# Kernel optimization log

Hardware: AMD Instinct MI355X
Metric: run time of the kernel (lower is better)

Reference implementation:

```python
import jax, jax.numpy as jnp
import numpy as np

# Fixed architecture constants (hardcoded in PPGEncoder)
B_DEF, C_IN, L_SEQ = 64, 4, 256
H, N_STATE, N_BLOCKS = 4, 4, 2  # d_model, SSM state size, n_blocks


def _layernorm(v, scale, bias, eps=1e-5):
    mu = v.mean(-1, keepdims=True)
    var = v.var(-1, keepdims=True)
    return (v - mu) / jnp.sqrt(var + eps) * scale + bias


def _avgpool1d(v, out_size):
    # AdaptiveAvgPool1d where out_size divides L evenly -> block mean
    b, c, l = v.shape
    return v.reshape(b, c, out_size, l // out_size).mean(-1)


def setup_inputs() -> dict:
    key = jax.random.key(0)
    ks = iter(jax.random.split(key, 40))
    nrm = lambda shape, s=1.0: jax.random.normal(next(ks), shape, jnp.float32) * s
    inp = {
        "x": nrm((B_DEF, C_IN, L_SEQ)),
        # S4 encoder / decoder linears
        "enc_W": nrm((C_IN, H), 0.5), "enc_b": jnp.zeros((H,), jnp.float32),
        # per-block S4D params, stacked over blocks
        "ln_s": jnp.ones((N_BLOCKS, H), jnp.float32), "ln_b": jnp.zeros((N_BLOCKS, H), jnp.float32),
        "log_dt": jax.random.uniform(next(ks), (N_BLOCKS, H), jnp.float32,
                                      minval=float(np.log(1e-3)), maxval=float(np.log(1e-1))),
        "A_re": nrm((N_BLOCKS, H, N_STATE), 0.5),
        "A_im": jnp.tile(jnp.pi * jnp.arange(N_STATE, dtype=jnp.float32), (N_BLOCKS, H, 1)),
        "C_re": nrm((N_BLOCKS, H, N_STATE), 0.5), "C_im": nrm((N_BLOCKS, H, N_STATE), 0.5),
        "D": nrm((N_BLOCKS, H), 1.0),
        "out_W": nrm((N_BLOCKS, H, H), 0.5), "out_b": jnp.zeros((N_BLOCKS, H), jnp.float32),
        "dec_W": nrm((H, H), 0.5), "dec_b": jnp.zeros((H,), jnp.float32),
        # projection MLP: Linear(1856,1024) LN ReLU Linear(1024,4096) LN ReLU Unflatten(512,8) Linear(8,4096)
        "W1": nrm((1856, 1024), 0.02), "b1": jnp.zeros((1024,), jnp.float32),
        "g1": jnp.ones((1024,), jnp.float32), "be1": jnp.zeros((1024,), jnp.float32),
        "W2": nrm((1024, 4096), 0.02), "b2": jnp.zeros((4096,), jnp.float32),
        "g2": jnp.ones((4096,), jnp.float32), "be2": jnp.zeros((4096,), jnp.float32),
        "W3": nrm((8, 4096), 0.3), "b3": jnp.zeros((4096,), jnp.float32),
    }
    return inp


def _s4_model(x, enc_W, enc_b, ln_s, ln_b, log_dt, A_re, A_im, C_re, C_im, D,
              out_W, out_b, dec_W, dec_b):
    # x: [B, C_IN, L]; S4Model consumes [B, L, d_input]
    L = x.shape[-1]
    u = jnp.einsum('bcl,ch->blh', x, enc_W) + enc_b  # [B,L,H]
    t = jnp.arange(L, dtype=jnp.float32)
    for i in range(ln_s.shape[0]):
        z = _layernorm(u, ln_s[i], ln_b[i])          # prenorm
        zc = jnp.swapaxes(z, 1, 2)                   # [B,H,L]
        dt = jnp.exp(log_dt[i])                      # [H]
        A = -jnp.exp(A_re[i]) + 1j * A_im[i]         # stable diag SSM [H,N]
        dtA = A * dt[:, None]
        Bd = (jnp.exp(dtA) - 1.0) / A                # ZOH input discretization
        C = C_re[i] + 1j * C_im[i]
        vand = jnp.exp(dtA[:, :, None] * t)          # [H,N,L] Vandermonde
        K = 2.0 * jnp.real(jnp.einsum('hn,hnl->hl', C * Bd, vand))  # [H,L]
        # causal FFT convolution + skip D
        Uf = jnp.fft.rfft(zc, n=2 * L)
        Kf = jnp.fft.rfft(K, n=2 * L)
        y = jnp.fft.irfft(Uf * Kf, n=2 * L)[..., :L] + D[i][:, None] * zc
        y = jax.nn.gelu(y)
        y = jnp.einsum('bhl,hk->blk', y, out_W[i]) + out_b[i]
        u = u + y                                    # residual
    return u @ dec_W + dec_b                         # [B,L,H]


def reference(x, enc_W, enc_b, ln_s, ln_b, log_dt, A_re, A_im, C_re, C_im, D,
              out_W, out_b, dec_W, dec_b, W1, b1, g1, be1, W2, b2, g2, be2, W3, b3):
    b = x.shape[0]
    s4_out = _s4_model(x, enc_W, enc_b, ln_s, ln_b, log_dt, A_re, A_im,
                       C_re, C_im, D, out_W, out_b, dec_W, dec_b)  # [B,L,H]
    zc = jnp.swapaxes(s4_out, 1, 2)                  # [B,H,L]
    z16 = _avgpool1d(zc, 16)                         # [B,4,16]
    # FeaturePyramidPooling on raw x: sizes 64,128,256
    fpp = jnp.concatenate([_avgpool1d(x, 64), _avgpool1d(x, 128), _avgpool1d(x, 256)], axis=-1)
    combined = jnp.concatenate([z16.reshape(b, -1), fpp.reshape(b, -1)], axis=1)  # [B,1856]
    h = jax.nn.relu(_layernorm(combined @ W1 + b1, g1, be1))   # [B,1024] (dropout=eval identity)
    h = jax.nn.relu(_layernorm(h @ W2 + b2, g2, be2))          # [B,4096]
    h = h.reshape(b, 512, 8)
    return h @ W3 + b3                                         # [B,512,4096]
```

## Files before the change

### kernel.cpp

```cpp
#include <hip/hip_runtime.h>
#include <hip/hip_bf16.h>
#include <math.h>

#define BDEF 64
#define LSEQ 256
#define HD   4
#define NST  4
#define NBLK 2

typedef float nfloat4 __attribute__((ext_vector_type(4)));

__device__ inline void nt_store4(const float4 v, float* p) {
    nfloat4 nv = {v.x, v.y, v.z, v.w};
    __builtin_nontemporal_store(nv, (nfloat4*)p);
}

__global__ __launch_bounds__(256) void s4front(
    const float* __restrict__ x, const float* __restrict__ enc_W,
    const float* __restrict__ enc_b, const float* __restrict__ ln_s,
    const float* __restrict__ ln_b, const float* __restrict__ log_dt,
    const float* __restrict__ A_re, const float* __restrict__ A_im,
    const float* __restrict__ C_re, const float* __restrict__ C_im,
    const float* __restrict__ Dp, const float* __restrict__ out_W,
    const float* __restrict__ out_b, const float* __restrict__ dec_W,
    const float* __restrict__ dec_b, float* __restrict__ combined)
{
    const int b = blockIdx.x;
    const int l = threadIdx.x;
    __shared__ float Kl[NBLK][LSEQ][4];
    __shared__ float x_lds[4][256];
    __shared__ float z_lds[256][4];
    __shared__ float s4_lds[256][4];

    {
        const float t = (float)l;
        for (int i = 0; i < NBLK; ++i) {
            #pragma unroll
            for (int h = 0; h < HD; ++h) {
                float dt = expf(log_dt[i*HD + h]);
                float acc = 0.f;
                #pragma unroll
                for (int n = 0; n < NST; ++n) {
                    const int idx = (i*HD + h)*NST + n;
                    float ar = -expf(A_re[idx]);
                    float ai = A_im[idx];
                    float dr = ar*dt, di = ai*dt;
                    float er  = expf(dr);
                    float e1r = er*cosf(di) - 1.0f;
                    float e1i = er*sinf(di);
                    float inv = 1.0f/(ar*ar + ai*ai);
                    float bdr = (e1r*ar + e1i*ai)*inv;
                    float bdi = (e1i*ar - e1r*ai)*inv;
                    float cr = C_re[idx], ci = C_im[idx];
                    float cbr = cr*bdr - ci*bdi;
                    float cbi = cr*bdi + ci*bdr;
                    float em = expf(dr*t);
                    float vr = em*cosf(di*t);
                    float vi = em*sinf(di*t);
                    acc += cbr*vr - cbi*vi;
                }
                Kl[i][l][h] = 2.0f*acc;
            }
        }
    }

    #pragma unroll
    for (int c = 0; c < 4; ++c)
        x_lds[c][l] = x[(b*4 + c)*256 + l];

    float u[4];
    #pragma unroll
    for (int h = 0; h < 4; ++h) {
        float a = enc_b[h];
        #pragma unroll
        for (int c = 0; c < 4; ++c) a += x_lds[c][l]*enc_W[c*4 + h];
        u[h] = a;
    }
    __syncthreads();

    for (int i = 0; i < NBLK; ++i) {
        float mu = 0.25f*(u[0]+u[1]+u[2]+u[3]);
        float var = 0.f;
        #pragma unroll
        for (int h = 0; h < 4; ++h) { float d = u[h]-mu; var += d*d; }
        var *= 0.25f;
        float rs = rsqrtf(var + 1e-5f);
        float z[4];
        #pragma unroll
        for (int h = 0; h < 4; ++h)
            z[h] = (u[h]-mu)*rs*ln_s[i*4 + h] + ln_b[i*4 + h];
        *(float4*)&z_lds[l][0] = make_float4(z[0], z[1], z[2], z[3]);
        __syncthreads();

        float y0 = 0.f, y1 = 0.f, y2 = 0.f, y3 = 0.f;
        const int mlim = l | 63;
        #pragma unroll 4
        for (int m = 0; m <= mlim; ++m) {
            float4 kk = *(const float4*)&Kl[i][m][0];
            int p = (l - m) & 255;
            float4 zz = *(const float4*)&z_lds[p][0];
            if (m <= l) {
                y0 += kk.x*zz.x; y1 += kk.y*zz.y;
                y2 += kk.z*zz.z; y3 += kk.w*zz.w;
            }
        }
        float y[4] = {y0, y1, y2, y3};
        #pragma unroll
        for (int h = 0; h < 4; ++h) {
            float v = y[h] + Dp[i*4 + h]*z[h];
            float inner = 0.7978845608028654f*(v + 0.044715f*v*v*v);
            y[h] = 0.5f*v*(1.0f + tanhf(inner));
        }
        #pragma unroll
        for (int k = 0; k < 4; ++k) {
            float a = out_b[i*4 + k];
            #pragma unroll
            for (int h = 0; h < 4; ++h) a += y[h]*out_W[(i*4 + h)*4 + k];
            u[k] += a;
        }
        __syncthreads();
    }

    #pragma unroll
    for (int h = 0; h < 4; ++h) {
        float a = dec_b[h];
        #pragma unroll
        for (int k = 0; k < 4; ++k) a += u[k]*dec_W[k*4 + h];
        s4_lds[l][h] = a;
    }
    __syncthreads();

    float* cmb = combined + b*1856;
    if (l < 64) {
        int h = l >> 4, kk = l & 15;
        float a = 0.f;
        #pragma unroll
        for (int j = 0; j < 16; ++j) a += s4_lds[kk*16 + j][h];
        cmb[l] = a*(1.0f/16.0f);
    }
    for (int e = l; e < 1792; e += 256) {
        int c = e/448, jj = e%448;
        float v;
        if (jj < 64) {
            v = 0.25f*(x_lds[c][4*jj] + x_lds[c][4*jj+1] +
                       x_lds[c][4*jj+2] + x_lds[c][4*jj+3]);
        } else if (jj < 192) {
            int q = jj - 64;
            v = 0.5f*(x_lds[c][2*q] + x_lds[c][2*q+1]);
        } else {
            v = x_lds[c][jj - 192];
        }
        cmb[64 + e] = v;
    }
}

template<int NCOLS, int ASTRIDE, int KCH>
__global__ __launch_bounds__(256) void mlp_part(
    const float* __restrict__ A, const float* __restrict__ W,
    float* __restrict__ parts)
{
    __shared__ float At[64][KCH + 4];
    __shared__ float Wl[KCH][64];
    const int ks = blockIdx.x, k0 = ks*KCH;
    const int j0 = blockIdx.y*64;
    const int t  = threadIdx.x;

    {
        constexpr int AF4 = 64*KCH/4;
        constexpr int RF4 = KCH/4;
        #pragma unroll
        for (int f = t; f < AF4; f += 256) {
            const int row = f / RF4, c4 = f % RF4;
            *(float4*)&At[row][c4*4] =
                *(const float4*)(A + (size_t)row*ASTRIDE + k0 + c4*4);
        }
        constexpr int WF4 = KCH*16;
        #pragma unroll
        for (int f = t; f < WF4; f += 256) {
            const int row = f >> 4, c4 = f & 15;
            *(float4*)&Wl[row][c4*4] =
                *(const float4*)(W + (size_t)(k0 + row)*NCOLS + j0 + c4*4);
        }
    }
    __syncthreads();

    const int bi = t >> 4, ji = t & 15;
    const int br = bi*4;
    float4 acc0 = {0,0,0,0}, acc1 = {0,0,0,0}, acc2 = {0,0,0,0}, acc3 = {0,0,0,0};
    #pragma unroll 8
    for (int k = 0; k < KCH; ++k) {
        float4 wv = *(const float4*)&Wl[k][ji*4];
        float a0 = At[br+0][k], a1 = At[br+1][k];
        float a2 = At[br+2][k], a3 = At[br+3][k];
        acc0.x += a0*wv.x; acc0.y += a0*wv.y; acc0.z += a0*wv.z; acc0.w += a0*wv.w;
        acc1.x += a1*wv.x; acc1.y += a1*wv.y; acc1.z += a1*wv.z; acc1.w += a1*wv.w;
        acc2.x += a2*wv.x; acc2.y += a2*wv.y; acc2.z += a2*wv.z; acc2.w += a2*wv.w;
        acc3.x += a3*wv.x; acc3.y += a3*wv.y; acc3.z += a3*wv.z; acc3.w += a3*wv.w;
    }
    float* pbase = parts + (size_t)(ks*64 + br)*NCOLS + j0 + ji*4;
    *(float4*)(pbase)             = acc0;
    *(float4*)(pbase + NCOLS)     = acc1;
    *(float4*)(pbase + 2*NCOLS)   = acc2;
    *(float4*)(pbase + 3*NCOLS)   = acc3;
}

template<int N>
__global__ __launch_bounds__(256) void reduce_ln_relu(
    const float* __restrict__ parts, const float* __restrict__ bias,
    const float* __restrict__ g, const float* __restrict__ be,
    float* __restrict__ out, int KS)
{
    constexpr int NV = N/1024;
    const int b = blockIdx.x, t = threadIdx.x;
    float4 acc[NV];
    #pragma unroll
    for (int v = 0; v < NV; ++v)
        acc[v] = *(const float4*)(bias + v*1024 + t*4);
    for (int ks = 0; ks < KS; ++ks) {
        const float* p = parts + (size_t)(ks*64 + b)*N;
        #pragma unroll
        for (int v = 0; v < NV; ++v) {
            float4 q = *(const float4*)(p + v*1024 + t*4);
            acc[v].x += q.x; acc[v].y += q.y; acc[v].z += q.z; acc[v].w += q.w;
        }
    }
    float s = 0.f, s2 = 0.f;
    #pragma unroll
    for (int v = 0; v < NV; ++v) {
        s  += acc[v].x + acc[v].y + acc[v].z + acc[v].w;
        s2 += acc[v].x*acc[v].x + acc[v].y*acc[v].y +
              acc[v].z*acc[v].z + acc[v].w*acc[v].w;
    }
    #pragma unroll
    for (int off = 32; off > 0; off >>= 1) {
        s  += __shfl_down(s,  off);
        s2 += __shfl_down(s2, off);
    }
    __shared__ float red[2][4];
    const int w = t >> 6;
    if ((t & 63) == 0) { red[0][w] = s; red[1][w] = s2; }
    __syncthreads();
    float ts  = red[0][0] + red[0][1] + red[0][2] + red[0][3];
    float ts2 = red[1][0] + red[1][1] + red[1][2] + red[1][3];
    const float inv_n = 1.0f/(float)N;
    float mu  = ts*inv_n;
    float var = ts2*inv_n - mu*mu;
    float rs  = rsqrtf(var + 1e-5f);
    #pragma unroll
    for (int v = 0; v < NV; ++v) {
        const int j = v*1024 + t*4;
        float4 gv  = *(const float4*)(g + j);
        float4 bev = *(const float4*)(be + j);
        float4 o;
        o.x = fmaxf((acc[v].x - mu)*rs*gv.x + bev.x, 0.f);
        o.y = fmaxf((acc[v].y - mu)*rs*gv.y + bev.y, 0.f);
        o.z = fmaxf((acc[v].z - mu)*rs*gv.z + bev.z, 0.f);
        o.w = fmaxf((acc[v].w - mu)*rs*gv.w + bev.w, 0.f);
        *(float4*)(out + (size_t)b*N + j) = o;
    }
}

#define ROWS_D 64
__global__ __launch_bounds__(256) void final_mm(
    const float* __restrict__ h2, const float* __restrict__ W3,
    const float* __restrict__ b3, float* __restrict__ out)
{
    const int rg = blockIdx.x;
    const int js = blockIdx.y;
    const int t  = threadIdx.x;
    const int bs0 = rg*ROWS_D;
    const int j = js*1024 + t*4;
    float4 w[8];
    #pragma unroll
    for (int k = 0; k < 8; ++k) w[k] = *(const float4*)(W3 + k*4096 + j);
    const float4 bv = *(const float4*)(b3 + j);
    const float* __restrict__ hrow = h2 + (size_t)bs0*8;
    float* __restrict__ obase = out + (size_t)bs0*4096 + j;
    #pragma unroll 4
    for (int r = 0; r < ROWS_D; ++r) {
        float4 acc = bv;
        #pragma unroll
        for (int k = 0; k < 8; ++k) {
            const float hv = hrow[r*8 + k];
            acc.x += hv*w[k].x; acc.y += hv*w[k].y;
            acc.z += hv*w[k].z; acc.w += hv*w[k].w;
        }
        nt_store4(acc, obase + (size_t)r*4096);
    }
}

extern "C" void kernel_launch(void* const* d_in, const int* in_sizes, int n_in,
                              void* d_out, int out_size, void* d_ws, size_t ws_size,
                              hipStream_t stream) {
    const float* x      = (const float*)d_in[0];
    const float* enc_W  = (const float*)d_in[1];
    const float* enc_b  = (const float*)d_in[2];
    const float* ln_s   = (const float*)d_in[3];
    const float* ln_b   = (const float*)d_in[4];
    const float* log_dt = (const float*)d_in[5];
    const float* A_re   = (const float*)d_in[6];
    const float* A_im   = (const float*)d_in[7];
    const float* C_re   = (const float*)d_in[8];
    const float* C_im   = (const float*)d_in[9];
    const float* Dp     = (const float*)d_in[10];
    const float* out_W  = (const float*)d_in[11];
    const float* out_b  = (const float*)d_in[12];
    const float* dec_W  = (const float*)d_in[13];
    const float* dec_b  = (const float*)d_in[14];
    const float* W1     = (const float*)d_in[15];
    const float* b1     = (const float*)d_in[16];
    const float* g1     = (const float*)d_in[17];
    const float* be1    = (const float*)d_in[18];
    const float* W2     = (const float*)d_in[19];
    const float* b2     = (const float*)d_in[20];
    const float* g2     = (const float*)d_in[21];
    const float* be2    = (const float*)d_in[22];
    const float* W3     = (const float*)d_in[23];
    const float* b3     = (const float*)d_in[24];
    float* out = (float*)d_out;

    float* ws = (float*)d_ws;
    float* combined = ws;
    float* parts1   = combined + 64*1856;
    float* h1       = parts1 + 29*64*1024;
    float* parts2   = h1 + 64*1024;
    float* h2       = parts2 + 8*64*4096;

    s4front<<<64, 256, 0, stream>>>(x, enc_W, enc_b, ln_s, ln_b, log_dt,
                                    A_re, A_im, C_re, C_im, Dp,
                                    out_W, out_b, dec_W, dec_b, combined);
    mlp_part<1024,1856,64><<<dim3(29,16), 256, 0, stream>>>(combined, W1, parts1);
    reduce_ln_relu<1024><<<64, 256, 0, stream>>>(parts1, b1, g1, be1, h1, 29);
    mlp_part<4096,1024,128><<<dim3(8,64), 256, 0, stream>>>(h1, W2, parts2);
    reduce_ln_relu<4096><<<64, 256, 0, stream>>>(parts2, b2, g2, be2, h2, 8);
    final_mm<<<dim3(512,4), 256, 0, stream>>>(h2, W3, b3, out);
}
```

Before: 187.7 us.

## Fuse all stages into one cooperative persistent kernel with grid syncs

Replaces the six separate kernel launches with a single cooperative kernel of 512 blocks that runs the S4 front end, both MLP layers with their LayerNorm reductions, and the final projection as phases separated by grid.sync. The aim is to remove inter-kernel launch gaps and tail effects. The second matmul now uses 16 K-splits of 64 instead of 8 of 128, and the inner loops read float4 from LDS for both operands. A fallback to the multi-kernel path runs if occupancy or the cooperative launch fails. Risks are grid-sync overhead, phases where most blocks sit idle, and a larger parts2 buffer.

```diff
diff --git a/kernel.cpp b/kernel.cpp
--- a/kernel.cpp
+++ b/kernel.cpp
@@ -1,12 +1,8 @@
 #include <hip/hip_runtime.h>
-#include <hip/hip_bf16.h>
+#include <hip/hip_cooperative_groups.h>
 #include <math.h>
 
-#define BDEF 64
-#define LSEQ 256
-#define HD   4
-#define NST  4
-#define NBLK 2
+namespace cg = cooperative_groups;
 
 typedef float nfloat4 __attribute__((ext_vector_type(4)));
 
@@ -15,35 +11,38 @@
     __builtin_nontemporal_store(nv, (nfloat4*)p);
 }
 
-__global__ __launch_bounds__(256) void s4front(
-    const float* __restrict__ x, const float* __restrict__ enc_W,
-    const float* __restrict__ enc_b, const float* __restrict__ ln_s,
-    const float* __restrict__ ln_b, const float* __restrict__ log_dt,
-    const float* __restrict__ A_re, const float* __restrict__ A_im,
-    const float* __restrict__ C_re, const float* __restrict__ C_im,
-    const float* __restrict__ Dp, const float* __restrict__ out_W,
-    const float* __restrict__ out_b, const float* __restrict__ dec_W,
-    const float* __restrict__ dec_b, float* __restrict__ combined)
-{
-    const int b = blockIdx.x;
-    const int l = threadIdx.x;
-    __shared__ float Kl[NBLK][LSEQ][4];
-    __shared__ float x_lds[4][256];
-    __shared__ float z_lds[256][4];
-    __shared__ float s4_lds[256][4];
+struct KArgs {
+    const float *x, *enc_W, *enc_b, *ln_s, *ln_b, *log_dt, *A_re, *A_im,
+                *C_re, *C_im, *Dp, *out_W, *out_b, *dec_W, *dec_b,
+                *W1, *b1, *g1, *be1, *W2, *b2, *g2, *be2, *W3, *b3;
+    float *combined, *parts1, *h1, *parts2, *h2, *out;
+};
+
+#define ACCROW(accv, av)                                        \
+    accv.x += av.x*w0.x + av.y*w1.x + av.z*w2.x + av.w*w3.x;    \
+    accv.y += av.x*w0.y + av.y*w1.y + av.z*w2.y + av.w*w3.y;    \
+    accv.z += av.x*w0.z + av.y*w1.z + av.z*w2.z + av.w*w3.z;    \
+    accv.w += av.x*w0.w + av.y*w1.w + av.z*w2.w + av.w*w3.w;
+
+__device__ inline void s4_phase(const KArgs& a, int b, int l, float* smem)
+{
+    float* Kl  = smem;
+    float* xl  = smem + 2048;
+    float* zl  = smem + 3072;
+    float* s4l = smem + 4096;
 
     {
-        const float t = (float)l;
-        for (int i = 0; i < NBLK; ++i) {
+        const float tt = (float)l;
+        for (int i = 0; i < 2; ++i) {
             #pragma unroll
-            for (int h = 0; h < HD; ++h) {
-                float dt = expf(log_dt[i*HD + h]);
+            for (int h = 0; h < 4; ++h) {
+                float dt = expf(a.log_dt[i*4 + h]);
                 float acc = 0.f;
                 #pragma unroll
-                for (int n = 0; n < NST; ++n) {
-                    const int idx = (i*HD + h)*NST + n;
-                    float ar = -expf(A_re[idx]);
-                    float ai = A_im[idx];
+                for (int n = 0; n < 4; ++n) {
+                    const int idx = (i*4 + h)*4 + n;
+                    float ar = -expf(a.A_re[idx]);
+                    float ai = a.A_im[idx];
                     float dr = ar*dt, di = ai*dt;
                     float er  = expf(dr);
                     float e1r = er*cosf(di) - 1.0f;
@@ -51,34 +50,34 @@
                     float inv = 1.0f/(ar*ar + ai*ai);
                     float bdr = (e1r*ar + e1i*ai)*inv;
                     float bdi = (e1i*ar - e1r*ai)*inv;
-                    float cr = C_re[idx], ci = C_im[idx];
+                    float cr = a.C_re[idx], ci = a.C_im[idx];
                     float cbr = cr*bdr - ci*bdi;
                     float cbi = cr*bdi + ci*bdr;
-                    float em = expf(dr*t);
-                    float vr = em*cosf(di*t);
-                    float vi = em*sinf(di*t);
+                    float em = expf(dr*tt);
+                    float vr = em*cosf(di*tt);
+                    float vi = em*sinf(di*tt);
                     acc += cbr*vr - cbi*vi;
                 }
-                Kl[i][l][h] = 2.0f*acc;
+                Kl[(i*256 + l)*4 + h] = 2.0f*acc;
             }
         }
     }
 
     #pragma unroll
     for (int c = 0; c < 4; ++c)
-        x_lds[c][l] = x[(b*4 + c)*256 + l];
+        xl[c*256 + l] = a.x[(b*4 + c)*256 + l];
 
     float u[4];
     #pragma unroll
     for (int h = 0; h < 4; ++h) {
-        float a = enc_b[h];
-        #pragma unroll
-        for (int c = 0; c < 4; ++c) a += x_lds[c][l]*enc_W[c*4 + h];
-        u[h] = a;
-    }
-    __syncthreads();
-
-    for (int i = 0; i < NBLK; ++i) {
+        float acc = a.enc_b[h];
+        #pragma unroll
+        for (int c = 0; c < 4; ++c) acc += xl[c*256 + l]*a.enc_W[c*4 + h];
+        u[h] = acc;
+    }
+    __syncthreads();
+
+    for (int i = 0; i < 2; ++i) {
         float mu = 0.25f*(u[0]+u[1]+u[2]+u[3]);
         float var = 0.f;
         #pragma unroll
@@ -88,17 +87,17 @@
         float z[4];
         #pragma unroll
         for (int h = 0; h < 4; ++h)
-            z[h] = (u[h]-mu)*rs*ln_s[i*4 + h] + ln_b[i*4 + h];
-        *(float4*)&z_lds[l][0] = make_float4(z[0], z[1], z[2], z[3]);
+            z[h] = (u[h]-mu)*rs*a.ln_s[i*4 + h] + a.ln_b[i*4 + h];
+        *(float4*)&zl[l*4] = make_float4(z[0], z[1], z[2], z[3]);
         __syncthreads();
 
         float y0 = 0.f, y1 = 0.f, y2 = 0.f, y3 = 0.f;
         const int mlim = l | 63;
         #pragma unroll 4
         for (int m = 0; m <= mlim; ++m) {
-            float4 kk = *(const float4*)&Kl[i][m][0];
+            float4 kk = *(float4*)&Kl[(i*256 + m)*4];
             int p = (l - m) & 255;
-            float4 zz = *(const float4*)&z_lds[p][0];
+            float4 zz = *(float4*)&zl[p*4];
             if (m <= l) {
                 y0 += kk.x*zz.x; y1 += kk.y*zz.y;
                 y2 += kk.z*zz.z; y3 += kk.w*zz.w;
@@ -107,111 +106,105 @@
         float y[4] = {y0, y1, y2, y3};
         #pragma unroll
         for (int h = 0; h < 4; ++h) {
-            float v = y[h] + Dp[i*4 + h]*z[h];
+            float v = y[h] + a.Dp[i*4 + h]*z[h];
             float inner = 0.7978845608028654f*(v + 0.044715f*v*v*v);
             y[h] = 0.5f*v*(1.0f + tanhf(inner));
         }
         #pragma unroll
         for (int k = 0; k < 4; ++k) {
-            float a = out_b[i*4 + k];
+            float acc = a.out_b[i*4 + k];
             #pragma unroll
-            for (int h = 0; h < 4; ++h) a += y[h]*out_W[(i*4 + h)*4 + k];
-            u[k] += a;
+            for (int h = 0; h < 4; ++h) acc += y[h]*a.out_W[(i*4 + h)*4 + k];
+            u[k] += acc;
         }
         __syncthreads();
     }
 
     #pragma unroll
     for (int h = 0; h < 4; ++h) {
-        float a = dec_b[h];
-        #pragma unroll
-        for (int k = 0; k < 4; ++k) a += u[k]*dec_W[k*4 + h];
-        s4_lds[l][h] = a;
-    }
-    __syncthreads();
-
-    float* cmb = combined + b*1856;
+        float acc = a.dec_b[h];
+        #pragma unroll
+        for (int k = 0; k < 4; ++k) acc += u[k]*a.dec_W[k*4 + h];
+        s4l[l*4 + h] = acc;
+    }
+    __syncthreads();
+
+    float* cmb = a.combined + b*1856;
     if (l < 64) {
         int h = l >> 4, kk = l & 15;
-        float a = 0.f;
-        #pragma unroll
-        for (int j = 0; j < 16; ++j) a += s4_lds[kk*16 + j][h];
-        cmb[l] = a*(1.0f/16.0f);
+        float acc = 0.f;
+        #pragma unroll
+        for (int j = 0; j < 16; ++j) acc += s4l[(kk*16 + j)*4 + h];
+        cmb[l] = acc*(1.0f/16.0f);
     }
     for (int e = l; e < 1792; e += 256) {
         int c = e/448, jj = e%448;
         float v;
         if (jj < 64) {
-            v = 0.25f*(x_lds[c][4*jj] + x_lds[c][4*jj+1] +
-                       x_lds[c][4*jj+2] + x_lds[c][4*jj+3]);
+            v = 0.25f*(xl[c*256 + 4*jj] + xl[c*256 + 4*jj+1] +
+                       xl[c*256 + 4*jj+2] + xl[c*256 + 4*jj+3]);
         } else if (jj < 192) {
             int q = jj - 64;
-            v = 0.5f*(x_lds[c][2*q] + x_lds[c][2*q+1]);
+            v = 0.5f*(xl[c*256 + 2*q] + xl[c*256 + 2*q+1]);
         } else {
-            v = x_lds[c][jj - 192];
+            v = xl[c*256 + jj - 192];
         }
         cmb[64 + e] = v;
     }
 }
 
-template<int NCOLS, int ASTRIDE, int KCH>
-__global__ __launch_bounds__(256) void mlp_part(
-    const float* __restrict__ A, const float* __restrict__ W,
-    float* __restrict__ parts)
-{
-    __shared__ float At[64][KCH + 4];
-    __shared__ float Wl[KCH][64];
-    const int ks = blockIdx.x, k0 = ks*KCH;
-    const int j0 = blockIdx.y*64;
-    const int t  = threadIdx.x;
-
-    {
-        constexpr int AF4 = 64*KCH/4;
-        constexpr int RF4 = KCH/4;
-        #pragma unroll
-        for (int f = t; f < AF4; f += 256) {
-            const int row = f / RF4, c4 = f % RF4;
-            *(float4*)&At[row][c4*4] =
-                *(const float4*)(A + (size_t)row*ASTRIDE + k0 + c4*4);
-        }
-        constexpr int WF4 = KCH*16;
-        #pragma unroll
-        for (int f = t; f < WF4; f += 256) {
-            const int row = f >> 4, c4 = f & 15;
-            *(float4*)&Wl[row][c4*4] =
-                *(const float4*)(W + (size_t)(k0 + row)*NCOLS + j0 + c4*4);
-        }
-    }
-    __syncthreads();
-
-    const int bi = t >> 4, ji = t & 15;
-    const int br = bi*4;
-    float4 acc0 = {0,0,0,0}, acc1 = {0,0,0,0}, acc2 = {0,0,0,0}, acc3 = {0,0,0,0};
-    #pragma unroll 8
-    for (int k = 0; k < KCH; ++k) {
-        float4 wv = *(const float4*)&Wl[k][ji*4];
-        float a0 = At[br+0][k], a1 = At[br+1][k];
-        float a2 = At[br+2][k], a3 = At[br+3][k];
-        acc0.x += a0*wv.x; acc0.y += a0*wv.y; acc0.z += a0*wv.z; acc0.w += a0*wv.w;
-        acc1.x += a1*wv.x; acc1.y += a1*wv.y; acc1.z += a1*wv.z; acc1.w += a1*wv.w;
-        acc2.x += a2*wv.x; acc2.y += a2*wv.y; acc2.z += a2*wv.z; acc2.w += a2*wv.w;
-        acc3.x += a3*wv.x; acc3.y += a3*wv.y; acc3.z += a3*wv.z; acc3.w += a3*wv.w;
+template<int NCOLS, int ASTRIDE>
+__device__ inline void mlp_tile64(const float* __restrict__ A,
+                                  const float* __restrict__ W,
+                                  float* __restrict__ parts,
+                                  int ks, int jt, int t, float* smem)
+{
+    constexpr int KCH = 64, APAD = 68;
+    float* At = smem;
+    float* Wl = smem + 64*APAD;
+    const int k0 = ks*KCH, j0 = jt*64;
+    __syncthreads();
+    #pragma unroll
+    for (int f = t; f < 64*16; f += 256) {
+        const int row = f >> 4, c4 = f & 15;
+        *(float4*)&At[row*APAD + c4*4] =
+            *(const float4*)(A + (size_t)row*ASTRIDE + k0 + c4*4);
+    }
+    #pragma unroll
+    for (int f = t; f < KCH*16; f += 256) {
+        const int row = f >> 4, c4 = f & 15;
+        *(float4*)&Wl[row*64 + c4*4] =
+            *(const float4*)(W + (size_t)(k0 + row)*NCOLS + j0 + c4*4);
+    }
+    __syncthreads();
+    const int ji = t & 15, br = (t >> 4)*4;
+    float4 acc0={0,0,0,0}, acc1={0,0,0,0}, acc2={0,0,0,0}, acc3={0,0,0,0};
+    #pragma unroll 4
+    for (int k4 = 0; k4 < KCH; k4 += 4) {
+        float4 w0 = *(float4*)&Wl[(k4+0)*64 + ji*4];
+        float4 w1 = *(float4*)&Wl[(k4+1)*64 + ji*4];
+        float4 w2 = *(float4*)&Wl[(k4+2)*64 + ji*4];
+        float4 w3 = *(float4*)&Wl[(k4+3)*64 + ji*4];
+        float4 a0 = *(float4*)&At[(br+0)*APAD + k4];
+        float4 a1 = *(float4*)&At[(br+1)*APAD + k4];
+        float4 a2 = *(float4*)&At[(br+2)*APAD + k4];
+        float4 a3 = *(float4*)&At[(br+3)*APAD + k4];
+        ACCROW(acc0, a0) ACCROW(acc1, a1) ACCROW(acc2, a2) ACCROW(acc3, a3)
     }
     float* pbase = parts + (size_t)(ks*64 + br)*NCOLS + j0 + ji*4;
-    *(float4*)(pbase)             = acc0;
-    *(float4*)(pbase + NCOLS)     = acc1;
-    *(float4*)(pbase + 2*NCOLS)   = acc2;
-    *(float4*)(pbase + 3*NCOLS)   = acc3;
+    *(float4*)(pbase)           = acc0;
+    *(float4*)(pbase + NCOLS)   = acc1;
+    *(float4*)(pbase + 2*NCOLS) = acc2;
+    *(float4*)(pbase + 3*NCOLS) = acc3;
 }
 
 template<int N>
-__global__ __launch_bounds__(256) void reduce_ln_relu(
-    const float* __restrict__ parts, const float* __restrict__ bias,
-    const float* __restrict__ g, const float* __restrict__ be,
-    float* __restrict__ out, int KS)
+__device__ inline void reduce_ln_phase(const float* __restrict__ parts,
+    const float* __restrict__ bias, const float* __restrict__ g,
+    const float* __restrict__ be, float* __restrict__ out,
+    int KS, int b, int t, float* smem)
 {
     constexpr int NV = N/1024;
-    const int b = blockIdx.x, t = threadIdx.x;
     float4 acc[NV];
     #pragma unroll
     for (int v = 0; v < NV; ++v)
@@ -236,12 +229,12 @@
         s  += __shfl_down(s,  off);
         s2 += __shfl_down(s2, off);
     }
-    __shared__ float red[2][4];
+    __syncthreads();
     const int w = t >> 6;
-    if ((t & 63) == 0) { red[0][w] = s; red[1][w] = s2; }
-    __syncthreads();
-    float ts  = red[0][0] + red[0][1] + red[0][2] + red[0][3];
-    float ts2 = red[1][0] + red[1][1] + red[1][2] + red[1][3];
+    if ((t & 63) == 0) { smem[w] = s; smem[4 + w] = s2; }
+    __syncthreads();
+    float ts  = smem[0] + smem[1] + smem[2] + smem[3];
+    float ts2 = smem[4] + smem[5] + smem[6] + smem[7];
     const float inv_n = 1.0f/(float)N;
     float mu  = ts*inv_n;
     float var = ts2*inv_n - mu*mu;
@@ -260,15 +253,143 @@
     }
 }
 
-#define ROWS_D 64
+#define SMEM_F 8448
+
+__global__ __launch_bounds__(256, 2) void mega(KArgs a)
+{
+    __shared__ float smem[SMEM_F];
+    cg::grid_group grid = cg::this_grid();
+    const int blk = blockIdx.x;
+    const int t   = threadIdx.x;
+
+    if (blk < 64) s4_phase(a, blk, t, smem);
+    __threadfence();
+    grid.sync();
+
+    if (blk < 464)
+        mlp_tile64<1024, 1856>(a.combined, a.W1, a.parts1,
+                               blk % 29, blk / 29, t, smem);
+    __threadfence();
+    grid.sync();
+
+    if (blk < 64)
+        reduce_ln_phase<1024>(a.parts1, a.b1, a.g1, a.be1, a.h1, 29, blk, t, smem);
+    __threadfence();
+    grid.sync();
+
+    #pragma unroll
+    for (int it = 0; it < 2; ++it) {
+        const int tile = blk + it*512;
+        mlp_tile64<4096, 1024>(a.h1, a.W2, a.parts2,
+                               tile & 15, tile >> 4, t, smem);
+    }
+    __threadfence();
+    grid.sync();
+
+    if (blk < 64)
+        reduce_ln_phase<4096>(a.parts2, a.b2, a.g2, a.be2, a.h2, 16, blk, t, smem);
+    __threadfence();
+    grid.sync();
+
+    {
+        const int rg  = blk;
+        const int bs0 = rg*64;
+        float* h_lds = smem;
+        __syncthreads();
+        for (int e = t; e < 512; e += 256)
+            h_lds[e] = a.h2[(size_t)rg*512 + e];
+        __syncthreads();
+        for (int js = 0; js < 4; ++js) {
+            const int j = js*1024 + t*4;
+            float4 w[8];
+            #pragma unroll
+            for (int k = 0; k < 8; ++k)
+                w[k] = *(const float4*)(a.W3 + k*4096 + j);
+            const float4 bv = *(const float4*)(a.b3 + j);
+            float* __restrict__ obase = a.out + (size_t)bs0*4096 + j;
+            #pragma unroll 4
+            for (int r = 0; r < 64; ++r) {
+                float4 acc = bv;
+                #pragma unroll
+                for (int k = 0; k < 8; ++k) {
+                    const float hv = h_lds[r*8 + k];
+                    acc.x += hv*w[k].x; acc.y += hv*w[k].y;
+                    acc.z += hv*w[k].z; acc.w += hv*w[k].w;
+                }
+                nt_store4(acc, obase + (size_t)r*4096);
+            }
+        }
+    }
+}
+
+__global__ __launch_bounds__(256) void s4front(KArgs a)
+{
+    __shared__ float smem[5120];
+    s4_phase(a, blockIdx.x, threadIdx.x, smem);
+}
+
+template<int NCOLS, int ASTRIDE, int KCH>
+__global__ __launch_bounds__(256) void mlp_part(
+    const float* __restrict__ A, const float* __restrict__ W,
+    float* __restrict__ parts)
+{
+    __shared__ float At[64][KCH + 4];
+    __shared__ float Wl[KCH][64];
+    const int ks = blockIdx.x, k0 = ks*KCH;
+    const int j0 = blockIdx.y*64;
+    const int t  = threadIdx.x;
+    constexpr int AF4 = 64*KCH/4, RF4 = KCH/4;
+    #pragma unroll
+    for (int f = t; f < AF4; f += 256) {
+        const int row = f / RF4, c4 = f % RF4;
+        *(float4*)&At[row][c4*4] =
+            *(const float4*)(A + (size_t)row*ASTRIDE + k0 + c4*4);
+    }
+    constexpr int WF4 = KCH*16;
+    #pragma unroll
+    for (int f = t; f < WF4; f += 256) {
+        const int row = f >> 4, c4 = f & 15;
+        *(float4*)&Wl[row][c4*4] =
+            *(const float4*)(W + (size_t)(k0 + row)*NCOLS + j0 + c4*4);
+    }
+    __syncthreads();
+    const int ji = t & 15, br = (t >> 4)*4;
+    float4 acc0={0,0,0,0}, acc1={0,0,0,0}, acc2={0,0,0,0}, acc3={0,0,0,0};
+    #pragma unroll 4
+    for (int k4 = 0; k4 < KCH; k4 += 4) {
+        float4 w0 = *(float4*)&Wl[k4+0][ji*4];
+        float4 w1 = *(float4*)&Wl[k4+1][ji*4];
+        float4 w2 = *(float4*)&Wl[k4+2][ji*4];
+        float4 w3 = *(float4*)&Wl[k4+3][ji*4];
+        float4 a0 = *(float4*)&At[br+0][k4];
+        float4 a1 = *(float4*)&At[br+1][k4];
+        float4 a2 = *(float4*)&At[br+2][k4];
+        float4 a3 = *(float4*)&At[br+3][k4];
+        ACCROW(acc0, a0) ACCROW(acc1, a1) ACCROW(acc2, a2) ACCROW(acc3, a3)
+    }
+    float* pbase = parts + (size_t)(ks*64 + br)*NCOLS + j0 + ji*4;
+    *(float4*)(pbase)           = acc0;
+    *(float4*)(pbase + NCOLS)   = acc1;
+    *(float4*)(pbase + 2*NCOLS) = acc2;
+    *(float4*)(pbase + 3*NCOLS) = acc3;
+}
+
+template<int N>
+__global__ __launch_bounds__(256) void reduce_ln_relu(
+    const float* __restrict__ parts, const float* __restrict__ bias,
+    const float* __restrict__ g, const float* __restrict__ be,
+    float* __restrict__ out, int KS)
+{
+    __shared__ float smem[8];
+    reduce_ln_phase<N>(parts, bias, g, be, out, KS, blockIdx.x, threadIdx.x, smem);
+}
+
 __global__ __launch_bounds__(256) void final_mm(
     const float* __restrict__ h2, const float* __restrict__ W3,
     const float* __restrict__ b3, float* __restrict__ out)
 {
-    const int rg = blockIdx.x;
-    const int js = blockIdx.y;
-    const int t  = threadIdx.x;
-    const int bs0 = rg*ROWS_D;
+    const int rg = blockIdx.x, js = blockIdx.y, t = threadIdx.x;
+    const int bs0 = rg*64;
     const int j = js*1024 + t*4;
     float4 w[8];
     #pragma unroll
@@ -277,7 +398,7 @@
     const float* __restrict__ hrow = h2 + (size_t)bs0*8;
     float* __restrict__ obase = out + (size_t)bs0*4096 + j;
     #pragma unroll 4
-    for (int r = 0; r < ROWS_D; ++r) {
+    for (int r = 0; r < 64; ++r) {
         float4 acc = bv;
         #pragma unroll
         for (int k = 0; k < 8; ++k) {
@@ -292,46 +413,56 @@
 extern "C" void kernel_launch(void* const* d_in, const int* in_sizes, int n_in,
                               void* d_out, int out_size, void* d_ws, size_t ws_size,
                               hipStream_t stream) {
-    const float* x      = (const float*)d_in[0];
-    const float* enc_W  = (const float*)d_in[1];
-    const float* enc_b  = (const float*)d_in[2];
-    const float* ln_s   = (const float*)d_in[3];
-    const float* ln_b   = (const float*)d_in[4];
-    const float* log_dt = (const float*)d_in[5];
-    const float* A_re   = (const float*)d_in[6];
-    const float* A_im   = (const float*)d_in[7];
-    const float* C_re   = (const float*)d_in[8];
-    const float* C_im   = (const float*)d_in[9];
-    const float* Dp     = (const float*)d_in[10];
-    const float* out_W  = (const float*)d_in[11];
-    const float* out_b  = (const float*)d_in[12];
-    const float* dec_W  = (const float*)d_in[13];
-    const float* dec_b  = (const float*)d_in[14];
-    const float* W1     = (const float*)d_in[15];
-    const float* b1     = (const float*)d_in[16];
-    const float* g1     = (const float*)d_in[17];
-    const float* be1    = (const float*)d_in[18];
-    const float* W2     = (const float*)d_in[19];
-    const float* b2     = (const float*)d_in[20];
-    const float* g2     = (const float*)d_in[21];
-    const float* be2    = (const float*)d_in[22];
-    const float* W3     = (const float*)d_in[23];
-    const float* b3     = (const float*)d_in[24];
-    float* out = (float*)d_out;
+    KArgs a;
+    a.x      = (const float*)d_in[0];
+    a.enc_W  = (const float*)d_in[1];
+    a.enc_b  = (const float*)d_in[2];
+    a.ln_s   = (const float*)d_in[3];
+    a.ln_b   = (const float*)d_in[4];
+    a.log_dt = (const float*)d_in[5];
+    a.A_re   = (const float*)d_in[6];
+    a.A_im   = (const float*)d_in[7];
+    a.C_re   = (const float*)d_in[8];
+    a.C_im   = (const float*)d_in[9];
+    a.Dp     = (const float*)d_in[10];
+    a.out_W  = (const float*)d_in[11];
+    a.out_b  = (const float*)d_in[12];
+    a.dec_W  = (const float*)d_in[13];
+    a.dec_b  = (const float*)d_in[14];
+    a.W1     = (const float*)d_in[15];
+    a.b1     = (const float*)d_in[16];
+    a.g1     = (const float*)d_in[17];
+    a.be1    = (const float*)d_in[18];
+    a.W2     = (const float*)d_in[19];
+    a.b2     = (const float*)d_in[20];
+    a.g2     = (const float*)d_in[21];
+    a.be2    = (const float*)d_in[22];
+    a.W3     = (const float*)d_in[23];
+    a.b3     = (const float*)d_in[24];
 
     float* ws = (float*)d_ws;
-    float* combined = ws;
-    float* parts1   = combined + 64*1856;
-    float* h1       = parts1 + 29*64*1024;
-    float* parts2   = h1 + 64*1024;
-    float* h2       = parts2 + 8*64*4096;
-
-    s4front<<<64, 256, 0, stream>>>(x, enc_W, enc_b, ln_s, ln_b, log_dt,
-                                    A_re, A_im, C_re, C_im, Dp,
-                                    out_W, out_b, dec_W, dec_b, combined);
-    mlp_part<1024,1856,64><<<dim3(29,16), 256, 0, stream>>>(combined, W1, parts1);
-    reduce_ln_relu<1024><<<64, 256, 0, stream>>>(parts1, b1, g1, be1, h1, 29);
-    mlp_part<4096,1024,128><<<dim3(8,64), 256, 0, stream>>>(h1, W2, parts2);
-    reduce_ln_relu<4096><<<64, 256, 0, stream>>>(parts2, b2, g2, be2, h2, 8);
-    final_mm<<<dim3(512,4), 256, 0, stream>>>(h2, W3, b3, out);
-}
+    a.combined = ws;
+    a.parts1   = a.combined + 64*1856;
+    a.h1       = a.parts1 + 29*64*1024;
+    a.parts2   = a.h1 + 64*1024;
+    a.h2       = a.parts2 + 16*64*4096;
+    a.out      = (float*)d_out;
+
+    int nb = 0;
+    hipError_t qerr = hipOccupancyMaxActiveBlocksPerMultiprocessor(
+        &nb, reinterpret_cast<const void*>(&mega), 256, 0);
+    if (qerr == hipSuccess && nb >= 2) {
+        void* params[] = { (void*)&a };
+        hipError_t lerr = hipLaunchCooperativeKernel(
+            reinterpret_cast<void*>(&mega), dim3(512), dim3(256),
+            params, 0, stream);
+        if (lerr == hipSuccess) return;
+    }
+
+    s4front<<<64, 256, 0, stream>>>(a);
+    mlp_part<1024,1856,64><<<dim3(29,16), 256, 0, stream>>>(a.combined, a.W1, a.parts1);
+    reduce_ln_relu<1024><<<64, 256, 0, stream>>>(a.parts1, a.b1, a.g1, a.be1, a.h1, 29);
+    mlp_part<4096,1024,128><<<dim3(8,64), 256, 0, stream>>>(a.h1, a.W2, a.parts2);
+    reduce_ln_relu<4096><<<64, 256, 0, stream>>>(a.parts2, a.b2, a.g2, a.be2, a.h2, 8);
+    final_mm<<<dim3(512,4), 256, 0, stream>>>(a.h2, a.W3, a.b3, a.out);
+}
```

Result: slower. 650.2 us (+246.4%).

## Fuse final LayerNorm/ReLU into output matmul and vectorize MLP k-loop

Applied to the files above, without the earlier changes.

Removes the separate reduce_ln_relu launch for the second MLP layer. A new final_fused kernel reduces the split-K partial sums and computes the LayerNorm statistics itself, then feeds its 64 output rows to the Linear(8,4096) via wave readlane broadcasts. Each of the 512 blocks redundantly re-reduces a full 4096-wide row, and the grid is now 512 blocks instead of 2048. The output stores are no longer nontemporal. Separately, the mlp_part inner loop now steps k by 4, using float4 LDS reads of A to cut LDS instruction count.

```diff
diff --git a/kernel.cpp b/kernel.cpp
--- a/kernel.cpp
+++ b/kernel.cpp
@@ -10,10 +10,15 @@
 
 typedef float nfloat4 __attribute__((ext_vector_type(4)));
 
-__device__ inline void nt_store4(const float4 v, float* p) {
-    nfloat4 nv = {v.x, v.y, v.z, v.w};
-    __builtin_nontemporal_store(nv, (nfloat4*)p);
-}
+__device__ inline float lane_bcast(float v, int lane) {
+    return __int_as_float(__builtin_amdgcn_readlane(__float_as_int(v), lane));
+}
+
+#define ACCROW(accv, av)                                        \
+    accv.x += av.x*w0.x + av.y*w1.x + av.z*w2.x + av.w*w3.x;    \
+    accv.y += av.x*w0.y + av.y*w1.y + av.z*w2.y + av.w*w3.y;    \
+    accv.z += av.x*w0.z + av.y*w1.z + av.z*w2.z + av.w*w3.z;    \
+    accv.w += av.x*w0.w + av.y*w1.w + av.z*w2.w + av.w*w3.w;
 
 __global__ __launch_bounds__(256) void s4front(
     const float* __restrict__ x, const float* __restrict__ enc_W,
@@ -159,7 +164,8 @@
     const float* __restrict__ A, const float* __restrict__ W,
     float* __restrict__ parts)
 {
-    __shared__ float At[64][KCH + 4];
+    constexpr int APAD = KCH + 4;
+    __shared__ float At[64][APAD];
     __shared__ float Wl[KCH][64];
     const int ks = blockIdx.x, k0 = ks*KCH;
     const int j0 = blockIdx.y*64;
@@ -184,24 +190,25 @@
     }
     __syncthreads();
 
-    const int bi = t >> 4, ji = t & 15;
-    const int br = bi*4;
-    float4 acc0 = {0,0,0,0}, acc1 = {0,0,0,0}, acc2 = {0,0,0,0}, acc3 = {0,0,0,0};
-    #pragma unroll 8
-    for (int k = 0; k < KCH; ++k) {
-        float4 wv = *(const float4*)&Wl[k][ji*4];
-        float a0 = At[br+0][k], a1 = At[br+1][k];
-        float a2 = At[br+2][k], a3 = At[br+3][k];
-        acc0.x += a0*wv.x; acc0.y += a0*wv.y; acc0.z += a0*wv.z; acc0.w += a0*wv.w;
-        acc1.x += a1*wv.x; acc1.y += a1*wv.y; acc1.z += a1*wv.z; acc1.w += a1*wv.w;
-        acc2.x += a2*wv.x; acc2.y += a2*wv.y; acc2.z += a2*wv.z; acc2.w += a2*wv.w;
-        acc3.x += a3*wv.x; acc3.y += a3*wv.y; acc3.z += a3*wv.z; acc3.w += a3*wv.w;
+    const int ji = t & 15, br = (t >> 4)*4;
+    float4 acc0={0,0,0,0}, acc1={0,0,0,0}, acc2={0,0,0,0}, acc3={0,0,0,0};
+    #pragma unroll 4
+    for (int k4 = 0; k4 < KCH; k4 += 4) {
+        float4 w0 = *(float4*)&Wl[k4+0][ji*4];
+        float4 w1 = *(float4*)&Wl[k4+1][ji*4];
+        float4 w2 = *(float4*)&Wl[k4+2][ji*4];
+        float4 w3 = *(float4*)&Wl[k4+3][ji*4];
+        float4 a0 = *(float4*)&At[br+0][k4];
+        float4 a1 = *(float4*)&At[br+1][k4];
+        float4 a2 = *(float4*)&At[br+2][k4];
+        float4 a3 = *(float4*)&At[br+3][k4];
+        ACCROW(acc0, a0) ACCROW(acc1, a1) ACCROW(acc2, a2) ACCROW(acc3, a3)
     }
     float* pbase = parts + (size_t)(ks*64 + br)*NCOLS + j0 + ji*4;
-    *(float4*)(pbase)             = acc0;
-    *(float4*)(pbase + NCOLS)     = acc1;
-    *(float4*)(pbase + 2*NCOLS)   = acc2;
-    *(float4*)(pbase + 3*NCOLS)   = acc3;
+    *(float4*)(pbase)           = acc0;
+    *(float4*)(pbase + NCOLS)   = acc1;
+    *(float4*)(pbase + 2*NCOLS) = acc2;
+    *(float4*)(pbase + 3*NCOLS) = acc3;
 }
 
 template<int N>
@@ -260,32 +267,91 @@
     }
 }
 
-#define ROWS_D 64
-__global__ __launch_bounds__(256) void final_mm(
-    const float* __restrict__ h2, const float* __restrict__ W3,
-    const float* __restrict__ b3, float* __restrict__ out)
+__global__ __launch_bounds__(256) void final_fused(
+    const float* __restrict__ parts2, const float* __restrict__ b2,
+    const float* __restrict__ g2, const float* __restrict__ be2,
+    const float* __restrict__ W3, const float* __restrict__ b3,
+    float* __restrict__ out)
 {
     const int rg = blockIdx.x;
-    const int js = blockIdx.y;
     const int t  = threadIdx.x;
-    const int bs0 = rg*ROWS_D;
-    const int j = js*1024 + t*4;
-    float4 w[8];
-    #pragma unroll
-    for (int k = 0; k < 8; ++k) w[k] = *(const float4*)(W3 + k*4096 + j);
-    const float4 bv = *(const float4*)(b3 + j);
-    const float* __restrict__ hrow = h2 + (size_t)bs0*8;
-    float* __restrict__ obase = out + (size_t)bs0*4096 + j;
-    #pragma unroll 4
-    for (int r = 0; r < ROWS_D; ++r) {
-        float4 acc = bv;
-        #pragma unroll
-        for (int k = 0; k < 8; ++k) {
-            const float hv = hrow[r*8 + k];
-            acc.x += hv*w[k].x; acc.y += hv*w[k].y;
-            acc.z += hv*w[k].z; acc.w += hv*w[k].w;
-        }
-        nt_store4(acc, obase + (size_t)r*4096);
+    const int b  = rg >> 3;
+    const int cbase = (rg & 7)*512;
+    __shared__ float hrow_l[512];
+    __shared__ float red[2][4];
+
+    float4 vals[4];
+    float s = 0.f, s2 = 0.f;
+    #pragma unroll
+    for (int v = 0; v < 4; ++v) {
+        const int j = t*16 + v*4;
+        float4 acc = *(const float4*)(b2 + j);
+        #pragma unroll
+        for (int ks = 0; ks < 8; ++ks) {
+            float4 q = *(const float4*)(parts2 + (size_t)(ks*64 + b)*4096 + j);
+            acc.x += q.x; acc.y += q.y; acc.z += q.z; acc.w += q.w;
+        }
+        vals[v] = acc;
+        s  += acc.x + acc.y + acc.z + acc.w;
+        s2 += acc.x*acc.x + acc.y*acc.y + acc.z*acc.z + acc.w*acc.w;
+    }
+    #pragma unroll
+    for (int off = 32; off > 0; off >>= 1) {
+        s  += __shfl_down(s,  off);
+        s2 += __shfl_down(s2, off);
+    }
+    const int w = t >> 6;
+    if ((t & 63) == 0) { red[0][w] = s; red[1][w] = s2; }
+    __syncthreads();
+    float ts  = red[0][0] + red[0][1] + red[0][2] + red[0][3];
+    float ts2 = red[1][0] + red[1][1] + red[1][2] + red[1][3];
+    float mu  = ts*(1.0f/4096.0f);
+    float var = ts2*(1.0f/4096.0f) - mu*mu;
+    float rs  = rsqrtf(var + 1e-5f);
+    if (t >= (rg & 7)*32 && t < (rg & 7)*32 + 32) {
+        #pragma unroll
+        for (int v = 0; v < 4; ++v) {
+            const int j = t*16 + v*4;
+            float4 gv  = *(const float4*)(g2 + j);
+            float4 bev = *(const float4*)(be2 + j);
+            float4 o;
+            o.x = fmaxf((vals[v].x - mu)*rs*gv.x + bev.x, 0.f);
+            o.y = fmaxf((vals[v].y - mu)*rs*gv.y + bev.y, 0.f);
+            o.z = fmaxf((vals[v].z - mu)*rs*gv.z + bev.z, 0.f);
+            o.w = fmaxf((vals[v].w - mu)*rs*gv.w + bev.w, 0.f);
+            *(float4*)&hrow_l[j - cbase] = o;
+        }
+    }
+    __syncthreads();
+
+    const int lane = t & 63;
+    float hreg[8];
+    {
+        float4 ha = *(float4*)&hrow_l[lane*8];
+        float4 hb = *(float4*)&hrow_l[lane*8 + 4];
+        hreg[0]=ha.x; hreg[1]=ha.y; hreg[2]=ha.z; hreg[3]=ha.w;
+        hreg[4]=hb.x; hreg[5]=hb.y; hreg[6]=hb.z; hreg[7]=hb.w;
+    }
+    const int bs0 = rg*64;
+    for (int js = 0; js < 4; ++js) {
+        const int j = js*1024 + t*4;
+        float4 wv[8];
+        #pragma unroll
+        for (int k = 0; k < 8; ++k)
+            wv[k] = *(const float4*)(W3 + k*4096 + j);
+        const float4 bv = *(const float4*)(b3 + j);
+        float* __restrict__ obase = out + (size_t)bs0*4096 + j;
+        #pragma unroll 4
+        for (int r = 0; r < 64; ++r) {
+            float4 acc = bv;
+            #pragma unroll
+            for (int k = 0; k < 8; ++k) {
+                const float hv = lane_bcast(hreg[k], r);
+                acc.x += hv*wv[k].x; acc.y += hv*wv[k].y;
+                acc.z += hv*wv[k].z; acc.w += hv*wv[k].w;
+            }
+            *(float4*)(obase + (size_t)r*4096) = acc;
+        }
     }
 }
 
@@ -324,7 +390,6 @@
     float* parts1   = combined + 64*1856;
     float* h1       = parts1 + 29*64*1024;
     float* parts2   = h1 + 64*1024;
-    float* h2       = parts2 + 8*64*4096;
 
     s4front<<<64, 256, 0, stream>>>(x, enc_W, enc_b, ln_s, ln_b, log_dt,
                                     A_re, A_im, C_re, C_im, Dp,
@@ -332,6 +397,5 @@
     mlp_part<1024,1856,64><<<dim3(29,16), 256, 0, stream>>>(combined, W1, parts1);
     reduce_ln_relu<1024><<<64, 256, 0, stream>>>(parts1, b1, g1, be1, h1, 29);
     mlp_part<4096,1024,128><<<dim3(8,64), 256, 0, stream>>>(h1, W2, parts2);
-    reduce_ln_relu<4096><<<64, 256, 0, stream>>>(parts2, b2, g2, be2, h2, 8);
-    final_mm<<<dim3(512,4), 256, 0, stream>>>(h2, W3, b3, out);
-}
+    final_fused<<<512, 256, 0, stream>>>(parts2, b2, g2, be2, W3, b3, out);
+}
```

New measurement: 208.6 us. +11.1%, slower.
